# Performance work log

Hardware: AMD Instinct MI355X
Metric: run time of the kernel (lower is better)

The kernel has to match this reference:

```python
import jax, jax.numpy as jnp
import numpy as np

N_NODES = 100000
N_EDGES = 1600000
D_IN = 128
D_OUT = 128


def setup_inputs() -> dict:
    key = jax.random.key(0)
    k1, k2, k3 = jax.random.split(key, 3)
    input_matrix = jax.random.normal(k1, (N_NODES, D_IN), dtype=jnp.float32)
    adjacency_coo_matrix = jax.random.randint(k2, (2, N_EDGES), 0, N_NODES, dtype=jnp.int64)
    # xavier-uniform-like init for the projection weights
    limit = float(np.sqrt(6.0 / (D_IN + D_OUT)))
    W = jax.random.uniform(k3, (D_IN, D_OUT), minval=-limit, maxval=limit, dtype=jnp.float32)
    return {"input_matrix": input_matrix, "adjacency_coo_matrix": adjacency_coo_matrix, "W": W}


def reference(input_matrix, adjacency_coo_matrix, W):
    N = input_matrix.shape[0]
    # add self edges (i -> i) for every node
    self_idx = jnp.arange(N, dtype=adjacency_coo_matrix.dtype)
    src = jnp.concatenate([adjacency_coo_matrix[0], self_idx])  # segment ids (rows of output)
    nbr = jnp.concatenate([adjacency_coo_matrix[1], self_idx])  # gather indices
    # gather neighbor features: [E+N, d_in]
    neighbors = input_matrix[nbr]
    # scatter-mean over destination nodes
    summed = jax.ops.segment_sum(neighbors, src, num_segments=N)
    counts = jax.ops.segment_sum(jnp.ones((src.shape[0],), dtype=input_matrix.dtype), src, num_segments=N)
    mean = summed / counts[:, None]  # counts >= 1 thanks to self edges
    # linear projection
    return mean @ W
```

## Files before the change

### kernel.cpp

```cpp
#include <hip/hip_runtime.h>
#include <stdint.h>

#define DIM 128
#define SB 256

typedef unsigned short u16;
typedef unsigned int u32;
typedef __attribute__((ext_vector_type(8))) short short8;
typedef __attribute__((ext_vector_type(4))) float floatx4;
typedef __attribute__((ext_vector_type(4))) float nt_f32x4;

__device__ __forceinline__ u16 f2bf(float f) {
    u32 u = __float_as_uint(f);
    if ((u & 0x7fffffffu) > 0x7f800000u) return (u16)0x7fc0;
    return (u16)((u + 0x7fffu + ((u >> 16) & 1u)) >> 16);
}

__global__ void __launch_bounds__(256) k_wprep(const float* __restrict__ W,
                                               u16* __restrict__ Wbf,
                                               u16* __restrict__ Yzero) {
    int g = blockIdx.x * 256 + threadIdx.x;
    if (g < DIM * DIM) {
        int n = g >> 7, k = g & 127;
        Wbf[g] = f2bf(W[k * DIM + n]);
    }
    if (blockIdx.x == 0 && threadIdx.x < 32)
        ((ushort4*)Yzero)[threadIdx.x] = make_ushort4(0, 0, 0, 0);
}

__global__ void __launch_bounds__(512) k_gemm_y(const float4* __restrict__ X4,
                                                const u16* __restrict__ Wbf,
                                                u16* __restrict__ Ybf,
                                                int* __restrict__ cursor, int N) {
    __shared__ __align__(16) u16 wt[DIM * 136];
    int t = threadIdx.x;
    int g = blockIdx.x * 512 + t;
    if (g < N) cursor[g] = 0;
    for (int i = t; i < DIM * 16; i += 512) {
        int row = i >> 4, c8 = i & 15;
        *(short8*)&wt[row * 136 + c8 * 8] = *(const short8*)&Wbf[row * 128 + c8 * 8];
    }
    __syncthreads();
    int w = t >> 6, l = t & 63;
    int q = l >> 4, c = l & 15;
    int row0 = (blockIdx.x * 8 + w) * 16;
    size_t mr = (size_t)min(row0 + c, N - 1) * 32;
    float4 u[8];
    #pragma unroll
    for (int kt = 0; kt < 4; ++kt) {
        u[2 * kt]     = X4[mr + kt * 8 + q * 2];
        u[2 * kt + 1] = X4[mr + kt * 8 + q * 2 + 1];
    }
    floatx4 acc[8] = {};
    #pragma unroll
    for (int kt = 0; kt < 4; ++kt) {
        short8 a;
        float4 u0 = u[2 * kt], u1 = u[2 * kt + 1];
        a[0] = (short)f2bf(u0.x); a[1] = (short)f2bf(u0.y);
        a[2] = (short)f2bf(u0.z); a[3] = (short)f2bf(u0.w);
        a[4] = (short)f2bf(u1.x); a[5] = (short)f2bf(u1.y);
        a[6] = (short)f2bf(u1.z); a[7] = (short)f2bf(u1.w);
        #pragma unroll
        for (int nt = 0; nt < 8; ++nt) {
            short8 b = *(const short8*)&wt[(nt * 16 + c) * 136 + kt * 32 + q * 8];
            acc[nt] = __builtin_amdgcn_mfma_f32_16x16x32_bf16(a, b, acc[nt], 0, 0, 0);
        }
    }
    #pragma unroll
    for (int r = 0; r < 4; ++r) {
        int orow = row0 + q * 4 + r;
        if (orow < N) {
            u16* yrow = Ybf + (size_t)orow * DIM;
            #pragma unroll
            for (int nt = 0; nt < 8; ++nt)
                yrow[nt * 16 + c] = f2bf(acc[nt][r]);
        }
    }
}

__global__ void __launch_bounds__(256) k_scatter(const int* __restrict__ adj,
                                                 int* __restrict__ cursor,
                                                 int* __restrict__ slots,
                                                 int E, int N, int cap) {
    int r = blockIdx.x & 7;
    int sub = blockIdx.x >> 3;
    int nsub = gridDim.x >> 3;
    int lo = N / 8 * r + min(r, N % 8);
    int hi = lo + N / 8 + (r < N % 8 ? 1 : 0);
    const int4* v4 = (const int4*)adj;
    int npair = E >> 3;
    for (int p = sub * 256 + threadIdx.x; p < npair; p += nsub * 256) {
        int4 s0 = v4[2 * p];
        int4 s1 = v4[2 * p + 1];
        int e0 = p * 8;
        int nb[8];
        #pragma unroll
        for (int k = 0; k < 8; ++k) nb[k] = adj[E + e0 + k];
        int ds[8] = {s0.x, s0.y, s0.z, s0.w, s1.x, s1.y, s1.z, s1.w};
        int cc[8];
        #pragma unroll
        for (int k = 0; k < 8; ++k) {
            bool hit = (ds[k] >= lo) & (ds[k] < hi);
            cc[k] = hit ? atomicAdd(&cursor[ds[k]], 1) : cap;
        }
        #pragma unroll
        for (int k = 0; k < 8; ++k) {
            if (cc[k] < cap)
                slots[(size_t)ds[k] * cap + cc[k]] =
                    ((unsigned)nb[k] < (unsigned)N) ? nb[k] : 0;
        }
    }
    int tail = E & 7;
    if (sub == 0 && threadIdx.x < tail) {
        int e = (E & ~7) + threadIdx.x;
        int d = adj[e];
        if (d >= lo && d < hi) {
            int nbv = adj[E + e];
            int c = atomicAdd(&cursor[d], 1);
            if (c < cap) slots[(size_t)d * cap + c] = ((unsigned)nbv < (unsigned)N) ? nbv : 0;
        }
    }
}

__device__ __forceinline__ void agg_core(const uint4* __restrict__ Yb4,
                                         const int* __restrict__ lst, int deg,
                                         int wid, int grp, int sl, int N,
                                         float4* __restrict__ out4) {
    float acc[8];
    {
        int id0 = (grp == 0) ? wid : N;
        uint4 v = Yb4[(size_t)id0 * 16 + sl];
        u32 c0[4] = {v.x, v.y, v.z, v.w};
        #pragma unroll
        for (int k2 = 0; k2 < 4; ++k2) {
            acc[2 * k2]     = __uint_as_float(c0[k2] << 16);
            acc[2 * k2 + 1] = __uint_as_float(c0[k2] & 0xffff0000u);
        }
    }
    for (int base = 0; base < deg; base += 32) {
        int id[8];
        #pragma unroll
        for (int qi = 0; qi < 8; ++qi) {
            int ee = base + qi * 4 + grp;
            int t = __builtin_nontemporal_load(&lst[ee]);
            id[qi] = (ee < deg) ? t : N;
        }
        uint4 v[8];
        #pragma unroll
        for (int qi = 0; qi < 8; ++qi)
            v[qi] = Yb4[(size_t)id[qi] * 16 + sl];
        #pragma unroll
        for (int qi = 0; qi < 8; ++qi) {
            u32 c0[4] = {v[qi].x, v[qi].y, v[qi].z, v[qi].w};
            #pragma unroll
            for (int k2 = 0; k2 < 4; ++k2) {
                acc[2 * k2]     += __uint_as_float(c0[k2] << 16);
                acc[2 * k2 + 1] += __uint_as_float(c0[k2] & 0xffff0000u);
            }
        }
    }
    #pragma unroll
    for (int j = 0; j < 8; ++j) {
        acc[j] += __shfl_xor(acc[j], 16);
        acc[j] += __shfl_xor(acc[j], 32);
    }
    float inv = 1.0f / (float)(deg + 1);
    if (grp < 2) {
        nt_f32x4 o;
        o.x = acc[grp * 4 + 0] * inv; o.y = acc[grp * 4 + 1] * inv;
        o.z = acc[grp * 4 + 2] * inv; o.w = acc[grp * 4 + 3] * inv;
        __builtin_nontemporal_store(o, (nt_f32x4*)&out4[(size_t)wid * 32 + sl * 2 + grp]);
    }
}

__global__ void __launch_bounds__(256) k_agg_cap(const uint4* __restrict__ Yb4,
                                                 const int* __restrict__ cnt,
                                                 const int* __restrict__ slots,
                                                 float4* __restrict__ out4, int N, int cap) {
    int wid = (blockIdx.x * 256 + threadIdx.x) >> 6;
    int lane = threadIdx.x & 63;
    if (wid >= N) return;
    int deg = min(cnt[wid], cap);
    agg_core(Yb4, slots + (size_t)wid * cap, deg, wid, lane >> 4, lane & 15, N, out4);
}

__global__ void __launch_bounds__(256) k_agg_off(const uint4* __restrict__ Yb4,
                                                 const int* __restrict__ offsets,
                                                 const int* __restrict__ sorted_nbr,
                                                 float4* __restrict__ out4, int N) {
    int wid = (blockIdx.x * 256 + threadIdx.x) >> 6;
    int lane = threadIdx.x & 63;
    if (wid >= N) return;
    int beg = offsets[wid], end = offsets[wid + 1];
    agg_core(Yb4, sorted_nbr + beg, end - beg, wid, lane >> 4, lane & 15, N, out4);
}

__global__ void __launch_bounds__(256) k_hist(const int* __restrict__ adj,
                                              int* __restrict__ counts, int E, int N) {
    int r = blockIdx.x & 7;
    int sub = blockIdx.x >> 3;
    int nsub = gridDim.x >> 3;
    int lo = N / 8 * r + min(r, N % 8);
    int hi = lo + N / 8 + (r < N % 8 ? 1 : 0);
    for (int e = sub * 256 + threadIdx.x; e < E; e += nsub * 256) {
        int d = adj[e];
        if (d >= lo && d < hi) atomicAdd(&counts[d], 1);
    }
}

__global__ void __launch_bounds__(SB) k_bsum(const int* __restrict__ counts,
                                             int* __restrict__ partials, int N) {
    __shared__ int lds[SB];
    int t = threadIdx.x;
    int i = blockIdx.x * SB + t;
    lds[t] = (i < N) ? counts[i] : 0;
    __syncthreads();
    for (int off = SB / 2; off > 0; off >>= 1) {
        if (t < off) lds[t] += lds[t + off];
        __syncthreads();
    }
    if (t == 0) partials[blockIdx.x] = lds[0];
}

__global__ void __launch_bounds__(1024) k_pscan(int* __restrict__ partials,
                                                int* __restrict__ offsets, int nb, int N) {
    __shared__ int lds[1024];
    int t = threadIdx.x;
    int v0 = (t < nb) ? partials[t] : 0;
    lds[t] = v0;
    __syncthreads();
    for (int off = 1; off < 1024; off <<= 1) {
        int v = (t >= off) ? lds[t - off] : 0;
        __syncthreads();
        lds[t] += v;
        __syncthreads();
    }
    if (t < nb) partials[t] = lds[t] - v0;
    if (t == 1023) offsets[N] = lds[1023];
}

__global__ void __launch_bounds__(SB) k_scan_final(const int* __restrict__ counts_in,
                                                   const int* __restrict__ partials,
                                                   int* __restrict__ offsets,
                                                   int* __restrict__ cursor, int N) {
    __shared__ int lds[SB];
    int t = threadIdx.x;
    int i = blockIdx.x * SB + t;
    int c = (i < N) ? counts_in[i] : 0;
    lds[t] = c;
    __syncthreads();
    for (int off = 1; off < SB; off <<= 1) {
        int v = (t >= off) ? lds[t - off] : 0;
        __syncthreads();
        lds[t] += v;
        __syncthreads();
    }
    int excl = lds[t] - c + partials[blockIdx.x];
    if (i < N) {
        offsets[i] = excl;
        cursor[i] = excl;
    }
}

__global__ void __launch_bounds__(256) k_reorder(const int* __restrict__ adj,
                                                 int* __restrict__ cursor,
                                                 int* __restrict__ sorted_nbr, int E, int N) {
    int r = blockIdx.x & 7;
    int sub = blockIdx.x >> 3;
    int nsub = gridDim.x >> 3;
    int lo = N / 8 * r + min(r, N % 8);
    int hi = lo + N / 8 + (r < N % 8 ? 1 : 0);
    for (int e = sub * 256 + threadIdx.x; e < E; e += nsub * 256) {
        int d = adj[e];
        if (d < lo || d >= hi) continue;
        int nb = adj[E + e];
        int pos = atomicAdd(&cursor[d], 1);
        sorted_nbr[pos] = ((unsigned)nb < (unsigned)N) ? nb : 0;
    }
}

extern "C" void kernel_launch(void* const* d_in, const int* in_sizes, int n_in,
                              void* d_out, int out_size, void* d_ws, size_t ws_size,
                              hipStream_t stream) {
    int N = in_sizes[0] / DIM;
    int E = in_sizes[1] / 2;
    const float* X = (const float*)d_in[0];
    const int* adj = (const int*)d_in[1];
    const float* W = (const float*)d_in[2];
    float* out = (float*)d_out;

    int gemm_blocks = (N + 127) / 128;
    size_t cur_b  = (size_t)N * 4;
    size_t y_b    = ((size_t)N + 1) * DIM * 2;
    size_t wbf_b  = (size_t)DIM * DIM * 2;

    int cap = 0;
    if (ws_size >= cur_b + (size_t)N * 64 * 4 + y_b + wbf_b) cap = 64;
    else if (ws_size >= cur_b + (size_t)N * 48 * 4 + y_b + wbf_b) cap = 48;

    if (cap) {
        int* cursor = (int*)d_ws;
        int* slots  = cursor + N;
        u16* Ybf    = (u16*)(slots + (size_t)N * cap);
        u16* Wbf    = Ybf + ((size_t)N + 1) * DIM;

        k_wprep<<<64, 256, 0, stream>>>(W, Wbf, Ybf + (size_t)N * DIM);
        k_gemm_y<<<gemm_blocks, 512, 0, stream>>>((const float4*)X, Wbf, Ybf, cursor, N);
        k_scatter<<<2048, 256, 0, stream>>>(adj, cursor, slots, E, N, cap);
        k_agg_cap<<<(N + 3) / 4, 256, 0, stream>>>((const uint4*)Ybf, cursor, slots,
                                                   (float4*)out, N, cap);
    } else {
        int nb = (N + SB - 1) / SB;
        int* cursor     = (int*)d_ws;
        int* offsets    = cursor + N;
        int* sorted_nbr = offsets + (N + 1);
        int* partials   = sorted_nbr + E;
        u16* Ybf        = (u16*)(partials + 512);
        u16* Wbf        = Ybf + ((size_t)N + 1) * DIM;

        k_wprep<<<64, 256, 0, stream>>>(W, Wbf, Ybf + (size_t)N * DIM);
        k_gemm_y<<<gemm_blocks, 512, 0, stream>>>((const float4*)X, Wbf, Ybf, cursor, N);
        k_hist<<<1024, 256, 0, stream>>>(adj, cursor, E, N);
        k_bsum<<<nb, SB, 0, stream>>>(cursor, partials, N);
        k_pscan<<<1, 1024, 0, stream>>>(partials, offsets, nb, N);
        k_scan_final<<<nb, SB, 0, stream>>>(cursor, partials, offsets, cursor, N);
        k_reorder<<<1024, 256, 0, stream>>>(adj, cursor, sorted_nbr, E, N);
        k_agg_off<<<(N + 3) / 4, 256, 0, stream>>>((const uint4*)Ybf, offsets, sorted_nbr,
                                                   (float4*)out, N);
    }
}
```

Measured before the change: 246.5 us.

## Fuse GEMM and edge scatter into one interleaved launch; move cursor zeroing

The bf16 projection GEMM and the bucketed edge-scatter now run as one kernel, with blocks interleaved by a proportional map so GEMM blocks and scatter blocks share the GPU at the same time. Cursor zeroing moves into the weight-prep kernel, which now launches enough blocks to cover N and so finishes before the fused kernel starts its atomics. The aim is to overlap the compute-bound GEMM with the atomic- and memory-bound scatter and to drop one launch. In exchange, scatter blocks now take 512 threads handling one chunk each instead of grid-striding, and every block reserves the GEMM's shared memory, which may lower occupancy for the scatter blocks.

```diff
diff --git a/kernel.cpp b/kernel.cpp
--- a/kernel.cpp
+++ b/kernel.cpp
@@ -18,106 +18,112 @@
 
 __global__ void __launch_bounds__(256) k_wprep(const float* __restrict__ W,
                                                u16* __restrict__ Wbf,
-                                               u16* __restrict__ Yzero) {
+                                               u16* __restrict__ Yzero,
+                                               int* __restrict__ cursor, int N) {
     int g = blockIdx.x * 256 + threadIdx.x;
     if (g < DIM * DIM) {
         int n = g >> 7, k = g & 127;
         Wbf[g] = f2bf(W[k * DIM + n]);
     }
+    if (g < N) cursor[g] = 0;
     if (blockIdx.x == 0 && threadIdx.x < 32)
         ((ushort4*)Yzero)[threadIdx.x] = make_ushort4(0, 0, 0, 0);
 }
 
-__global__ void __launch_bounds__(512) k_gemm_y(const float4* __restrict__ X4,
-                                                const u16* __restrict__ Wbf,
-                                                u16* __restrict__ Ybf,
-                                                int* __restrict__ cursor, int N) {
+__global__ void __launch_bounds__(512) k_fused(const float4* __restrict__ X4,
+                                               const u16* __restrict__ Wbf,
+                                               u16* __restrict__ Ybf,
+                                               const int* __restrict__ adj,
+                                               int* __restrict__ cursor,
+                                               int* __restrict__ slots,
+                                               int E, int N, int cap, int G, int T) {
     __shared__ __align__(16) u16 wt[DIM * 136];
-    int t = threadIdx.x;
-    int g = blockIdx.x * 512 + t;
-    if (g < N) cursor[g] = 0;
-    for (int i = t; i < DIM * 16; i += 512) {
-        int row = i >> 4, c8 = i & 15;
-        *(short8*)&wt[row * 136 + c8 * 8] = *(const short8*)&Wbf[row * 128 + c8 * 8];
-    }
-    __syncthreads();
-    int w = t >> 6, l = t & 63;
-    int q = l >> 4, c = l & 15;
-    int row0 = (blockIdx.x * 8 + w) * 16;
-    size_t mr = (size_t)min(row0 + c, N - 1) * 32;
-    float4 u[8];
-    #pragma unroll
-    for (int kt = 0; kt < 4; ++kt) {
-        u[2 * kt]     = X4[mr + kt * 8 + q * 2];
-        u[2 * kt + 1] = X4[mr + kt * 8 + q * 2 + 1];
-    }
-    floatx4 acc[8] = {};
-    #pragma unroll
-    for (int kt = 0; kt < 4; ++kt) {
-        short8 a;
-        float4 u0 = u[2 * kt], u1 = u[2 * kt + 1];
-        a[0] = (short)f2bf(u0.x); a[1] = (short)f2bf(u0.y);
-        a[2] = (short)f2bf(u0.z); a[3] = (short)f2bf(u0.w);
-        a[4] = (short)f2bf(u1.x); a[5] = (short)f2bf(u1.y);
-        a[6] = (short)f2bf(u1.z); a[7] = (short)f2bf(u1.w);
-        #pragma unroll
-        for (int nt = 0; nt < 8; ++nt) {
-            short8 b = *(const short8*)&wt[(nt * 16 + c) * 136 + kt * 32 + q * 8];
-            acc[nt] = __builtin_amdgcn_mfma_f32_16x16x32_bf16(a, b, acc[nt], 0, 0, 0);
-        }
-    }
-    #pragma unroll
-    for (int r = 0; r < 4; ++r) {
-        int orow = row0 + q * 4 + r;
-        if (orow < N) {
-            u16* yrow = Ybf + (size_t)orow * DIM;
-            #pragma unroll
-            for (int nt = 0; nt < 8; ++nt)
-                yrow[nt * 16 + c] = f2bf(acc[nt][r]);
-        }
-    }
-}
-
-__global__ void __launch_bounds__(256) k_scatter(const int* __restrict__ adj,
-                                                 int* __restrict__ cursor,
-                                                 int* __restrict__ slots,
-                                                 int E, int N, int cap) {
-    int r = blockIdx.x & 7;
-    int sub = blockIdx.x >> 3;
-    int nsub = gridDim.x >> 3;
-    int lo = N / 8 * r + min(r, N % 8);
-    int hi = lo + N / 8 + (r < N % 8 ? 1 : 0);
-    const int4* v4 = (const int4*)adj;
-    int npair = E >> 3;
-    for (int p = sub * 256 + threadIdx.x; p < npair; p += nsub * 256) {
-        int4 s0 = v4[2 * p];
-        int4 s1 = v4[2 * p + 1];
-        int e0 = p * 8;
-        int nb[8];
-        #pragma unroll
-        for (int k = 0; k < 8; ++k) nb[k] = adj[E + e0 + k];
-        int ds[8] = {s0.x, s0.y, s0.z, s0.w, s1.x, s1.y, s1.z, s1.w};
-        int cc[8];
-        #pragma unroll
-        for (int k = 0; k < 8; ++k) {
-            bool hit = (ds[k] >= lo) & (ds[k] < hi);
-            cc[k] = hit ? atomicAdd(&cursor[ds[k]], 1) : cap;
-        }
-        #pragma unroll
-        for (int k = 0; k < 8; ++k) {
-            if (cc[k] < cap)
-                slots[(size_t)ds[k] * cap + cc[k]] =
-                    ((unsigned)nb[k] < (unsigned)N) ? nb[k] : 0;
-        }
-    }
-    int tail = E & 7;
-    if (sub == 0 && threadIdx.x < tail) {
-        int e = (E & ~7) + threadIdx.x;
-        int d = adj[e];
-        if (d >= lo && d < hi) {
-            int nbv = adj[E + e];
-            int c = atomicAdd(&cursor[d], 1);
-            if (c < cap) slots[(size_t)d * cap + c] = ((unsigned)nbv < (unsigned)N) ? nbv : 0;
+    int b = blockIdx.x;
+    long a0 = ((long)b * G) / T;
+    long a1 = ((long)(b + 1) * G) / T;
+    if (a1 > a0) {
+        int gb = (int)a0;
+        int t = threadIdx.x;
+        for (int i = t; i < DIM * 16; i += 512) {
+            int row = i >> 4, c8 = i & 15;
+            *(short8*)&wt[row * 136 + c8 * 8] = *(const short8*)&Wbf[row * 128 + c8 * 8];
+        }
+        __syncthreads();
+        int w = t >> 6, l = t & 63;
+        int q = l >> 4, c = l & 15;
+        int row0 = (gb * 8 + w) * 16;
+        size_t mr = (size_t)min(row0 + c, N - 1) * 32;
+        float4 u[8];
+        #pragma unroll
+        for (int kt = 0; kt < 4; ++kt) {
+            u[2 * kt]     = X4[mr + kt * 8 + q * 2];
+            u[2 * kt + 1] = X4[mr + kt * 8 + q * 2 + 1];
+        }
+        floatx4 acc[8] = {};
+        #pragma unroll
+        for (int kt = 0; kt < 4; ++kt) {
+            short8 a;
+            float4 u0 = u[2 * kt], u1 = u[2 * kt + 1];
+            a[0] = (short)f2bf(u0.x); a[1] = (short)f2bf(u0.y);
+            a[2] = (short)f2bf(u0.z); a[3] = (short)f2bf(u0.w);
+            a[4] = (short)f2bf(u1.x); a[5] = (short)f2bf(u1.y);
+            a[6] = (short)f2bf(u1.z); a[7] = (short)f2bf(u1.w);
+            #pragma unroll
+            for (int nt = 0; nt < 8; ++nt) {
+                short8 bb = *(const short8*)&wt[(nt * 16 + c) * 136 + kt * 32 + q * 8];
+                acc[nt] = __builtin_amdgcn_mfma_f32_16x16x32_bf16(a, bb, acc[nt], 0, 0, 0);
+            }
+        }
+        #pragma unroll
+        for (int r = 0; r < 4; ++r) {
+            int orow = row0 + q * 4 + r;
+            if (orow < N) {
+                u16* yrow = Ybf + (size_t)orow * DIM;
+                #pragma unroll
+                for (int nt = 0; nt < 8; ++nt)
+                    yrow[nt * 16 + c] = f2bf(acc[nt][r]);
+            }
+        }
+    } else {
+        int sid = b - (int)a1;
+        int r = sid & 7;
+        int sub = sid >> 3;
+        int lo = N / 8 * r + min(r, N % 8);
+        int hi = lo + N / 8 + (r < N % 8 ? 1 : 0);
+        const int4* v4 = (const int4*)adj;
+        int npair = E >> 3;
+        int p = sub * 512 + threadIdx.x;
+        if (p < npair) {
+            int4 s0 = v4[2 * p];
+            int4 s1 = v4[2 * p + 1];
+            int e0 = p * 8;
+            int nb[8];
+            #pragma unroll
+            for (int k = 0; k < 8; ++k) nb[k] = adj[E + e0 + k];
+            int ds[8] = {s0.x, s0.y, s0.z, s0.w, s1.x, s1.y, s1.z, s1.w};
+            int cc[8];
+            #pragma unroll
+            for (int k = 0; k < 8; ++k) {
+                bool hit = (ds[k] >= lo) & (ds[k] < hi);
+                cc[k] = hit ? atomicAdd(&cursor[ds[k]], 1) : cap;
+            }
+            #pragma unroll
+            for (int k = 0; k < 8; ++k) {
+                if (cc[k] < cap)
+                    slots[(size_t)ds[k] * cap + cc[k]] =
+                        ((unsigned)nb[k] < (unsigned)N) ? nb[k] : 0;
+            }
+        }
+        int tail = E & 7;
+        if (sub == 0 && threadIdx.x < tail) {
+            int e = (E & ~7) + threadIdx.x;
+            int d = adj[e];
+            if (d >= lo && d < hi) {
+                int nbv = adj[E + e];
+                int c = atomicAdd(&cursor[d], 1);
+                if (c < cap)
+                    slots[(size_t)d * cap + c] = ((unsigned)nbv < (unsigned)N) ? nbv : 0;
+            }
         }
     }
 }
@@ -289,7 +295,13 @@
     const float* W = (const float*)d_in[2];
     float* out = (float*)d_out;
 
-    int gemm_blocks = (N + 127) / 128;
+    int G = (N + 127) / 128;
+    int npair = E >> 3;
+    int S = 8 * ((npair + 511) / 512);
+    int T = G + S;
+
+    int wprep_blocks = (N + 255) / 256;
+
     size_t cur_b  = (size_t)N * 4;
     size_t y_b    = ((size_t)N + 1) * DIM * 2;
     size_t wbf_b  = (size_t)DIM * DIM * 2;
@@ -304,9 +316,9 @@
         u16* Ybf    = (u16*)(slots + (size_t)N * cap);
         u16* Wbf    = Ybf + ((size_t)N + 1) * DIM;
 
-        k_wprep<<<64, 256, 0, stream>>>(W, Wbf, Ybf + (size_t)N * DIM);
-        k_gemm_y<<<gemm_blocks, 512, 0, stream>>>((const float4*)X, Wbf, Ybf, cursor, N);
-        k_scatter<<<2048, 256, 0, stream>>>(adj, cursor, slots, E, N, cap);
+        k_wprep<<<wprep_blocks, 256, 0, stream>>>(W, Wbf, Ybf + (size_t)N * DIM, cursor, N);
+        k_fused<<<T, 512, 0, stream>>>((const float4*)X, Wbf, Ybf, adj, cursor, slots,
+                                       E, N, cap, G, T);
         k_agg_cap<<<(N + 3) / 4, 256, 0, stream>>>((const uint4*)Ybf, cursor, slots,
                                                    (float4*)out, N, cap);
     } else {
@@ -318,8 +330,9 @@
         u16* Ybf        = (u16*)(partials + 512);
         u16* Wbf        = Ybf + ((size_t)N + 1) * DIM;
 
-        k_wprep<<<64, 256, 0, stream>>>(W, Wbf, Ybf + (size_t)N * DIM);
-        k_gemm_y<<<gemm_blocks, 512, 0, stream>>>((const float4*)X, Wbf, Ybf, cursor, N);
+        k_wprep<<<wprep_blocks, 256, 0, stream>>>(W, Wbf, Ybf + (size_t)N * DIM, cursor, N);
+        k_fused<<<G, 512, 0, stream>>>((const float4*)X, Wbf, Ybf, adj, cursor, nullptr,
+                                       E, N, 0, G, G);
         k_hist<<<1024, 256, 0, stream>>>(adj, cursor, E, N);
         k_bsum<<<nb, SB, 0, stream>>>(cursor, partials, N);
         k_pscan<<<1, 1024, 0, stream>>>(partials, offsets, nb, N);
```

Result: faster. 232.8 us (-5.5%).
